# Kernel optimization log

Hardware: AMD Instinct MI355X
Metric: run time of the kernel (lower is better)

Reference implementation:

```python
import jax, jax.numpy as jnp
import numpy as np

B, M, N = 32, 512, 512
XD = YD = 512   # x_size, y_size
S = 512         # shared_size
H = 512         # hidden_size
MAXD = 11       # max relative distance


def _lin(k, i, o):
    lim = float(np.sqrt(6.0 / (i + o)))  # xavier_uniform, gain=1
    return jax.random.uniform(k, (i, o), jnp.float32, -lim, lim)


def setup_inputs() -> dict:
    key = jax.random.key(0)
    ks = jax.random.split(key, 16)
    inp = {
        'prem': jax.random.normal(ks[0], (B, M, YD), jnp.float32),
        'hypo': jax.random.normal(ks[1], (B, N, XD), jnp.float32),
        'prem_mask': jnp.ones((B, M), dtype=bool),
        'hypo_mask': jnp.ones((B, N), dtype=bool),
        # projections
        'Wpx': _lin(ks[2], XD, S), 'bpx': jnp.zeros((S,), jnp.float32),
        'Wpy': _lin(ks[3], YD, S), 'bpy': jnp.zeros((S,), jnp.float32),
        # relative-distance bias embedding (2*max_dist+1, squeezed to scalar)
        'dist_embed': jax.random.normal(ks[4], (2 * MAXD + 1,), jnp.float32),
        # self-attention DeepDot MLP: S -> H -> H
        'Ws1': _lin(ks[5], S, H), 'bs1': jnp.zeros((H,), jnp.float32),
        'Ws2': _lin(ks[6], H, H), 'bs2': jnp.zeros((H,), jnp.float32),
        # cross-attention DeepDot MLP: 2S -> H -> H
        'Wa1': _lin(ks[7], 2 * S, H), 'ba1': jnp.zeros((H,), jnp.float32),
        'Wa2': _lin(ks[8], H, H), 'ba2': jnp.zeros((H,), jnp.float32),
        # compare layer: 4S -> H -> H
        'Wc1': _lin(ks[9], 4 * S, H), 'bc1': jnp.zeros((H,), jnp.float32),
        'Wc2': _lin(ks[10], H, H), 'bc2': jnp.zeros((H,), jnp.float32),
        # aggregate layer: 2H -> H -> H
        'Wg1': _lin(ks[11], 2 * H, H), 'bg1': jnp.zeros((H,), jnp.float32),
        'Wg2': _lin(ks[12], H, H), 'bg2': jnp.zeros((H,), jnp.float32),
    }
    return inp


def _mlp2(x, W1, b1, W2, b2):
    # Linear -> ReLU -> Linear -> ReLU (dropout=0.0)
    h = jax.nn.relu(x @ W1 + b1)
    return jax.nn.relu(h @ W2 + b2)


def _rel_bias(size, dist_embed):
    v = jnp.arange(size)
    d = jnp.clip(v[None, :] - v[:, None], -MAXD, MAXD) + MAXD  # [size,size]
    return dist_embed[d]


def _masked_softmax(t, mask):
    # mask True = valid; broadcast over query dim
    return jax.nn.softmax(jnp.where(mask, t, -jnp.inf), axis=-1)


def reference(prem, hypo, prem_mask, hypo_mask,
              Wpx, bpx, Wpy, bpy, dist_embed,
              Ws1, bs1, Ws2, bs2,
              Wa1, ba1, Wa2, ba2,
              Wc1, bc1, Wc2, bc2,
              Wg1, bg1, Wg2, bg2):
    hypo_p = hypo @ Wpx + bpx   # [B,N,S]
    prem_p = prem @ Wpy + bpy   # [B,M,S]

    # self attention (DeepDot: shared MLP on q and k, then qk^T)
    fp = _mlp2(prem_p, Ws1, bs1, Ws2, bs2)
    fh = _mlp2(hypo_p, Ws1, bs1, Ws2, bs2)
    p_scores = jnp.einsum('bmh,bnh->bmn', fp, fp) + _rel_bias(prem_p.shape[1], dist_embed)[None]
    h_scores = jnp.einsum('bmh,bnh->bmn', fh, fh) + _rel_bias(hypo_p.shape[1], dist_embed)[None]

    p_att = _masked_softmax(p_scores, prem_mask[:, None, :])
    h_att = _masked_softmax(h_scores, hypo_mask[:, None, :])
    prem_ctx = jnp.einsum('bmn,bnd->bmd', p_att, prem_p)
    hypo_ctx = jnp.einsum('bmn,bnd->bmd', h_att, hypo_p)

    prem2 = jnp.concatenate([prem_p, prem_ctx], axis=-1)  # [B,M,2S]
    hypo2 = jnp.concatenate([hypo_p, hypo_ctx], axis=-1)  # [B,N,2S]

    # cross attention
    gp = _mlp2(prem2, Wa1, ba1, Wa2, ba2)
    gh = _mlp2(hypo2, Wa1, ba1, Wa2, ba2)
    sim = jnp.einsum('bmh,bnh->bmn', gp, gh)  # [B,M,N]
    p2h = _masked_softmax(sim, hypo_mask[:, None, :])
    h2p = _masked_softmax(jnp.swapaxes(sim, 1, 2), prem_mask[:, None, :])
    attended_hypo = jnp.einsum('bmn,bnd->bmd', p2h, hypo2)  # [B,M,2S]
    attended_prem = jnp.einsum('bnm,bmd->bnd', h2p, prem2)  # [B,N,2S]

    prem_cmp = _mlp2(jnp.concatenate([prem2, attended_hypo], -1), Wc1, bc1, Wc2, bc2)
    hypo_cmp = _mlp2(jnp.concatenate([hypo2, attended_prem], -1), Wc1, bc1, Wc2, bc2)

    prem_cmp = (prem_cmp * prem_mask[..., None].astype(prem_cmp.dtype)).sum(axis=1)  # [B,H]
    hypo_cmp = (hypo_cmp * hypo_mask[..., None].astype(hypo_cmp.dtype)).sum(axis=1)  # [B,H]

    return _mlp2(jnp.concatenate([prem_cmp, hypo_cmp], -1), Wg1, bg1, Wg2, bg2)
```

## Files before the change

kernel.cpp:

```cpp
#include <hip/hip_runtime.h>
#include <hip/hip_bf16.h>


typedef __bf16 bf16x8 __attribute__((ext_vector_type(8)));
typedef float floatx16 __attribute__((ext_vector_type(16)));
typedef float floatx4 __attribute__((ext_vector_type(4)));

__device__ __forceinline__ unsigned short f32_to_bf16(float f) {
    unsigned int u = __float_as_uint(f);
    unsigned int r = (u + 0x7FFFu + ((u >> 16) & 1u)) >> 16;
    return (unsigned short)r;
}
__device__ __forceinline__ float bf16_to_f32(unsigned short h) {
    return __uint_as_float(((unsigned int)h) << 16);
}

__device__ __forceinline__ void gload16(const void* g, void* l) {
    __builtin_amdgcn_global_load_lds(
        (const __attribute__((address_space(1))) unsigned int*)g,
        (__attribute__((address_space(3))) unsigned int*)l, 16, 0, 0);
}

#define FENCE_BAR() do { asm volatile("" ::: "memory"); \
    __builtin_amdgcn_s_barrier(); \
    asm volatile("" ::: "memory"); } while (0)

struct TW {
    const float* src[8];
    unsigned short* dst[8];
    int K[8];
};
__global__ __launch_bounds__(256) void transpose_all_kernel(TW tw) {
    const int z = blockIdx.z;
    const int K = tw.K[z];
    const int k0 = blockIdx.y * 32;
    if (k0 >= K) return;
    const float* W = tw.src[z];
    unsigned short* Wt = tw.dst[z];
    __shared__ unsigned short tile[32][33];
    int n0 = blockIdx.x * 32;
    int tx = threadIdx.x & 31, ty = threadIdx.x >> 5;
    #pragma unroll
    for (int i = 0; i < 4; ++i) {
        int ky = ty + i * 8;
        tile[ky][tx] = f32_to_bf16(W[(long long)(k0 + ky) * 512 + n0 + tx]);
    }
    __syncthreads();
    #pragma unroll
    for (int i = 0; i < 4; ++i) {
        int ny = ty + i * 8;
        Wt[(long long)(n0 + ny) * K + k0 + tx] = tile[tx][ny];
    }
}

template <bool BT, bool AF32>
__global__ __launch_bounds__(256, 4) void gemm_kernel(
    const void* __restrict__ Av, const void* __restrict__ A2v, int lda, long long strideA,
    const unsigned short* __restrict__ Bw, int ldb, long long strideB, int bxor,
    const unsigned short* __restrict__ B2, const float* __restrict__ bias2, int Msplit,
    float* __restrict__ C32, unsigned short* __restrict__ Cb, int ldc, long long strideC,
    const float* __restrict__ bias, int relu, int M, int N, int K,
    float* __restrict__ csum, int swz) {
    constexpr int BBYTES = BT ? 8192 : (32 * 264);
    constexpr int BUF = 8192 + BBYTES;
    __shared__ alignas(16) char smem[2 * BUF];

    const int t = threadIdx.x;
    const int lane = t & 63;
    const int wave = t >> 6;
    const int wm = (wave >> 1) * 64;
    const int wn = (wave & 1) * 64;
    const int ln = lane & 31;
    const int h = lane >> 5;

    int bx = blockIdx.x, by = blockIdx.y, bz = blockIdx.z;
    if (swz == 1) {
        int Nt = gridDim.x, Mt = gridDim.y;
        int L = by * Nt + bx;
        int x = L & 7, s = L >> 3;
        by = x * (Mt >> 3) + s / Nt;
        bx = s % Nt;
    } else if (swz == 2) {
        int Nt = gridDim.x, Mt = gridDim.y;
        int L = (bz * Mt + by) * Nt + bx;
        int x = L & 7, s = L >> 3;
        int mg = x * ((Mt * (int)gridDim.z) >> 3) + s / Nt;
        bx = s % Nt;
        by = mg % Mt;
        bz = mg / Mt;
    }
    const int m0 = by * 128;
    const int n0 = bx * 128;
    const int bzB = (bz + bxor) & ((int)gridDim.z - 1);

    const unsigned short* B = Bw;
    const float* biasp = bias;
    long long mA = m0;
    if (Msplit && m0 >= Msplit) {
        if (B2) B = B2;
        if (bias2) biasp = bias2;
        if (A2v) { Av = A2v; mA = m0 - Msplit; }
    }

    const float* aptrF = nullptr;
    const unsigned short* aptrH = nullptr;
    if constexpr (AF32)
        aptrF = (const float*)Av + (long long)bz * strideA +
                (mA + (t >> 1)) * (long long)lda + (t & 1) * 16;
    else
        aptrH = (const unsigned short*)Av + (long long)bz * strideA +
                (mA + (t >> 1)) * (long long)lda + (t & 1) * 16;
    const unsigned short* bptr;
    if (BT)
        bptr = B + (long long)bzB * strideB +
               (long long)(n0 + (t >> 1)) * ldb + (t & 1) * 16;
    else
        bptr = B + (long long)bzB * strideB +
               (long long)(t >> 4) * ldb + n0 + (t & 15) * 8;
    const long long bstep = BT ? 8 : 16 * (long long)ldb;

    const int aoff = ((t & 1) * 256 + (t >> 1)) * 16;
    const int boff = BT ? (8192 + ((t & 1) * 256 + (t >> 1)) * 16)
                        : (8192 + (t >> 4) * 264 + (t & 15) * 16);
    const int boff2 = BT ? 2048 : 16 * 264;

    floatx16 acc[2][2];
    #pragma unroll
    for (int im = 0; im < 2; ++im)
        #pragma unroll
        for (int in = 0; in < 2; ++in)
            acc[im][in] = (floatx16)(0.f);

    uint4 va0, va1, vb0, vb1;
    float4 fa0, fa1, fa2, fa3;

    auto loadA = [&]() {
        if constexpr (AF32) {
            fa0 = *(const float4*)(aptrF);
            fa1 = *(const float4*)(aptrF + 4);
            fa2 = *(const float4*)(aptrF + 8);
            fa3 = *(const float4*)(aptrF + 12);
            aptrF += 32;
        } else {
            va0 = *(const uint4*)(aptrH);
            va1 = *(const uint4*)(aptrH + 8);
            aptrH += 32;
        }
    };
    auto loadB = [&]() {
        vb0 = *(const uint4*)(bptr);
        vb1 = *(const uint4*)(bptr + bstep);
        bptr += BT ? 32 : 32 * (long long)ldb;
    };
    auto commit = [&](char* buf) {
        if constexpr (AF32) {
            union { uint4 q; unsigned short u[8]; } c0, c1;
            c0.u[0] = f32_to_bf16(fa0.x); c0.u[1] = f32_to_bf16(fa0.y);
            c0.u[2] = f32_to_bf16(fa0.z); c0.u[3] = f32_to_bf16(fa0.w);
            c0.u[4] = f32_to_bf16(fa1.x); c0.u[5] = f32_to_bf16(fa1.y);
            c0.u[6] = f32_to_bf16(fa1.z); c0.u[7] = f32_to_bf16(fa1.w);
            c1.u[0] = f32_to_bf16(fa2.x); c1.u[1] = f32_to_bf16(fa2.y);
            c1.u[2] = f32_to_bf16(fa2.z); c1.u[3] = f32_to_bf16(fa2.w);
            c1.u[4] = f32_to_bf16(fa3.x); c1.u[5] = f32_to_bf16(fa3.y);
            c1.u[6] = f32_to_bf16(fa3.z); c1.u[7] = f32_to_bf16(fa3.w);
            *(uint4*)(buf + aoff) = c0.q;
            *(uint4*)(buf + aoff + 2048) = c1.q;
        } else {
            *(uint4*)(buf + aoff) = va0;
            *(uint4*)(buf + aoff + 2048) = va1;
        }
        *(uint4*)(buf + boff) = vb0;
        *(uint4*)(buf + boff + boff2) = vb1;
    };

    loadA(); loadB();
    commit(smem);
    loadA(); loadB();
    __syncthreads();

    int p = 0;
    for (int k0 = 0; k0 < K; k0 += 32) {
        const char* base = smem + p * BUF;
        #pragma unroll
        for (int s = 0; s < 2; ++s) {
            bf16x8 a[2], b[2];
            #pragma unroll
            for (int im = 0; im < 2; ++im)
                a[im] = *(const bf16x8*)(base + ((s * 2 + h) * 128 + wm + im * 32 + ln) * 16);
            if (BT) {
                #pragma unroll
                for (int in = 0; in < 2; ++in)
                    b[in] = *(const bf16x8*)(base + 8192 +
                                             ((s * 2 + h) * 128 + wn + in * 32 + ln) * 16);
            } else {
                #pragma unroll
                for (int in = 0; in < 2; ++in) {
                    union { bf16x8 v; unsigned short u[8]; } u;
                    #pragma unroll
                    for (int j = 0; j < 8; ++j)
                        u.u[j] = *(const unsigned short*)(base + 8192 +
                                 (s * 16 + h * 8 + j) * 264 + (wn + in * 32 + ln) * 2);
                    b[in] = u.v;
                }
            }
            #pragma unroll
            for (int im = 0; im < 2; ++im)
                #pragma unroll
                for (int in = 0; in < 2; ++in)
                    acc[im][in] = __builtin_amdgcn_mfma_f32_32x32x16_bf16(
                        a[im], b[in], acc[im][in], 0, 0, 0);
        }

        if (k0 + 32 < K) {
            commit(smem + (p ^ 1) * BUF);
            if (k0 + 64 < K) { loadA(); loadB(); }
            __syncthreads();
            p ^= 1;
        }
    }

    if (csum) {
        const int bidx = m0 >> 9;
        const long long cbase = (long long)(bidx & 31) * 1024 + (bidx >> 5) * 512;
        #pragma unroll
        for (int in = 0; in < 2; ++in) {
            int n = n0 + wn + in * 32 + ln;
            float bn = biasp ? biasp[n] : 0.f;
            float s = 0.f;
            #pragma unroll
            for (int im = 0; im < 2; ++im)
                #pragma unroll
                for (int r = 0; r < 16; ++r) {
                    float v = acc[im][in][r] + bn;
                    if (relu) v = fmaxf(v, 0.f);
                    s += v;
                }
            s += __shfl_xor(s, 32);
            if (lane < 32) atomicAdd(&csum[cbase + n], s);
        }
        return;
    }

    float* C32b = C32 ? C32 + (long long)bz * strideC : nullptr;
    unsigned short* Cbb = Cb ? Cb + (long long)bz * strideC : nullptr;
    #pragma unroll
    for (int im = 0; im < 2; ++im) {
        #pragma unroll
        for (int in = 0; in < 2; ++in) {
            int n = n0 + wn + in * 32 + ln;
            float bn = biasp ? biasp[n] : 0.f;
            #pragma unroll
            for (int r = 0; r < 16; ++r) {
                int m = m0 + wm + im * 32 + (r & 3) + 8 * (r >> 2) + 4 * h;
                float v = acc[im][in][r] + bn;
                if (relu) v = fmaxf(v, 0.f);
                long long off = (long long)m * ldc + n;
                if (C32b) C32b[off] = v;
                if (Cbb) Cbb[off] = f32_to_bf16(v);
            }
        }
    }
}

__global__ __launch_bounds__(512, 2) void gemm256_kernel(
    const unsigned short* __restrict__ Aw, int lda, long long strideA,
    const unsigned short* __restrict__ Bw, int ldb, long long strideB, int bxor,
    float* __restrict__ C32, unsigned short* __restrict__ Cb, int ldc, long long strideC,
    const float* __restrict__ bias, int relu, int K) {
    extern __shared__ __align__(16) char smem[];

    const int tid = threadIdx.x;
    const int lane = tid & 63;
    const int wave = tid >> 6;
    const int wr = wave >> 2;
    const int wc = wave & 3;

    int bx = blockIdx.x, by = blockIdx.y, bz = blockIdx.z;
    {
        const int gx = gridDim.x, gy = gridDim.y;
        const int nwg = gx * gy * (int)gridDim.z;
        if ((nwg & 7) == 0) {
            int L = (bz * gy + by) * gx + bx;
            int flat = (L & 7) * (nwg >> 3) + (L >> 3);
            bx = flat % gx;
            int R = flat / gx;
            by = R % gy;
            bz = R / gy;
        }
    }
    const int m0 = by * 256;
    const int n0 = bx * 256;
    const int bzB = (bz + bxor) & ((int)gridDim.z - 1);

    const int rowT = tid >> 3;
    const int chS = (tid & 7) ^ (rowT & 7);
    const long long ldaB = (long long)lda * 2;
    const long long ldbB = (long long)ldb * 2;
    const char* aG = (const char*)Aw +
        ((long long)bz * strideA + (long long)(m0 + rowT) * lda) * 2 + chS * 16;
    const char* bG = (const char*)Bw +
        ((long long)bzB * strideB + (long long)(n0 + rowT) * ldb) * 2 + chS * 16;
    const int dOff = tid * 16;

    auto stA = [&](int tt, int h) {
        const char* g = aG + (long long)(h * 128) * ldaB + (long long)tt * 128;
        char* l = smem + (tt & 1) * 65536 + h * 16384 + dOff;
        gload16(g, l);
        gload16(g + 64 * ldaB, l + 8192);
    };
    auto stB = [&](int tt, int h) {
        const char* g = bG + (long long)(h * 128) * ldbB + (long long)tt * 128;
        char* l = smem + (tt & 1) * 65536 + 32768 + h * 16384 + dOff;
        gload16(g, l);
        gload16(g + 64 * ldbB, l + 8192);
    };

    const int l15 = lane & 15;
    const int lk = lane >> 4;
    const int swzb = (lane & 7) << 4;
    const int c0 = (lk * 16) ^ swzb;
    const int c1 = (64 + lk * 16) ^ swzb;
    const int arow = (wr * 128 + l15) * 128;
    const int brow = 32768 + (wc * 64 + l15) * 128;

    floatx4 acc[8][4];
    #pragma unroll
    for (int mf = 0; mf < 8; ++mf)
        #pragma unroll
        for (int nf = 0; nf < 4; ++nf)
            acc[mf][nf] = (floatx4)(0.f);

    const int NT = K >> 6;

    stA(0, 0); stA(0, 1); stB(0, 0); stB(0, 1);
    if (NT > 1) {
        stB(1, 0); stB(1, 1);
        asm volatile("s_waitcnt vmcnt(4)" ::: "memory");
    } else {
        asm volatile("s_waitcnt vmcnt(0)" ::: "memory");
    }
    FENCE_BAR();

    bf16x8 a[4][2], b[4][2];
    for (int t = 0; t < NT; ++t) {
        const char* buf = smem + (t & 1) * 65536;
        const char* aB = buf + arow;
        const char* bB = buf + brow;

        #pragma unroll
        for (int mf = 0; mf < 4; ++mf) {
            a[mf][0] = *(const bf16x8*)(aB + mf * 2048 + c0);
            a[mf][1] = *(const bf16x8*)(aB + mf * 2048 + c1);
        }
        #pragma unroll
        for (int nf = 0; nf < 2; ++nf) {
            b[nf][0] = *(const bf16x8*)(bB + nf * 2048 + c0);
            b[nf][1] = *(const bf16x8*)(bB + nf * 2048 + c1);
        }
        if (t + 1 < NT) stA(t + 1, 0);
        FENCE_BAR();
        __builtin_amdgcn_s_setprio(1);
        #pragma unroll
        for (int mf = 0; mf < 4; ++mf)
            #pragma unroll
            for (int nf = 0; nf < 2; ++nf) {
                acc[mf][nf] = __builtin_amdgcn_mfma_f32_16x16x32_bf16(
                    a[mf][0], b[nf][0], acc[mf][nf], 0, 0, 0);
                acc[mf][nf] = __builtin_amdgcn_mfma_f32_16x16x32_bf16(
                    a[mf][1], b[nf][1], acc[mf][nf], 0, 0, 0);
            }
        __builtin_amdgcn_s_setprio(0);
        FENCE_BAR();

        #pragma unroll
        for (int nf = 2; nf < 4; ++nf) {
            b[nf][0] = *(const bf16x8*)(bB + nf * 2048 + c0);
            b[nf][1] = *(const bf16x8*)(bB + nf * 2048 + c1);
        }
        if (t + 1 < NT) stA(t + 1, 1);
        FENCE_BAR();
        __builtin_amdgcn_s_setprio(1);
        #pragma unroll
        for (int mf = 0; mf < 4; ++mf)
            #pragma unroll
            for (int nf = 2; nf < 4; ++nf) {
                acc[mf][nf] = __builtin_amdgcn_mfma_f32_16x16x32_bf16(
                    a[mf][0], b[nf][0], acc[mf][nf], 0, 0, 0);
                acc[mf][nf] = __builtin_amdgcn_mfma_f32_16x16x32_bf16(
                    a[mf][1], b[nf][1], acc[mf][nf], 0, 0, 0);
            }
        __builtin_amdgcn_s_setprio(0);
        FENCE_BAR();

        #pragma unroll
        for (int mf = 0; mf < 4; ++mf) {
            a[mf][0] = *(const bf16x8*)(aB + (4 + mf) * 2048 + c0);
            a[mf][1] = *(const bf16x8*)(aB + (4 + mf) * 2048 + c1);
        }
        if (t + 2 < NT) stB(t + 2, 0);
        FENCE_BAR();
        __builtin_amdgcn_s_setprio(1);
        #pragma unroll
        for (int mf = 0; mf < 4; ++mf)
            #pragma unroll
            for (int nf = 2; nf < 4; ++nf) {
                acc[4 + mf][nf] = __builtin_amdgcn_mfma_f32_16x16x32_bf16(
                    a[mf][0], b[nf][0], acc[4 + mf][nf], 0, 0, 0);
                acc[4 + mf][nf] = __builtin_amdgcn_mfma_f32_16x16x32_bf16(
                    a[mf][1], b[nf][1], acc[4 + mf][nf], 0, 0, 0);
            }
        __builtin_amdgcn_s_setprio(0);
        FENCE_BAR();

        if (t + 2 < NT) {
            stB(t + 2, 1);
            asm volatile("s_waitcnt vmcnt(4)" ::: "memory");
        } else {
            asm volatile("s_waitcnt vmcnt(0)" ::: "memory");
        }
        FENCE_BAR();
        __builtin_amdgcn_s_setprio(1);
        #pragma unroll
        for (int mf = 0; mf < 4; ++mf)
            #pragma unroll
            for (int nf = 0; nf < 2; ++nf) {
                acc[4 + mf][nf] = __builtin_amdgcn_mfma_f32_16x16x32_bf16(
                    a[mf][0], b[nf][0], acc[4 + mf][nf], 0, 0, 0);
                acc[4 + mf][nf] = __builtin_amdgcn_mfma_f32_16x16x32_bf16(
                    a[mf][1], b[nf][1], acc[4 + mf][nf], 0, 0, 0);
            }
        __builtin_amdgcn_s_setprio(0);
        FENCE_BAR();
    }

    const int rg = (lane >> 4) * 4;
    float* C32b = C32 ? C32 + (long long)bz * strideC : nullptr;
    unsigned short* Cbb = Cb ? Cb + (long long)bz * strideC : nullptr;
    #pragma unroll
    for (int nf = 0; nf < 4; ++nf) {
        const int n = n0 + wc * 64 + nf * 16 + l15;
        const float bn = bias ? bias[n] : 0.f;
        #pragma unroll
        for (int mf = 0; mf < 8; ++mf) {
            #pragma unroll
            for (int r = 0; r < 4; ++r) {
                int m = m0 + wr * 128 + mf * 16 + rg + r;
                float v = acc[mf][nf][r] + bn;
                if (relu) v = fmaxf(v, 0.f);
                long long off = (long long)m * ldc + n;
                if (C32b) C32b[off] = v;
                if (Cbb) Cbb[off] = f32_to_bf16(v);
            }
        }
    }
}

__global__ __launch_bounds__(256) void softmax_kernel(const float* S,
                                                      unsigned short* P,
                                                      const float* de, int rel) {
    const int row = blockIdx.x;
    const int b = blockIdx.y;
    const long long baseS = ((long long)b * 512 + row) * 512;
    const long long baseP = ((long long)b * 512 + row) * 1024;
    const int t = threadIdx.x;
    const int lane = t & 63, wv = t >> 6;
    __shared__ float redmax[4], redsum[4];

    float v[2];
    float mx = -1e30f;
    #pragma unroll
    for (int i = 0; i < 2; ++i) {
        int c = t + i * 256;
        float x = S[baseS + c];
        if (rel) {
            int d = c - row;
            d = min(11, max(-11, d));
            x += de[d + 11];
        }
        v[i] = x;
        mx = fmaxf(mx, x);
    }
    #pragma unroll
    for (int o = 32; o > 0; o >>= 1) mx = fmaxf(mx, __shfl_down(mx, o));
    if (lane == 0) redmax[wv] = mx;
    __syncthreads();
    mx = fmaxf(fmaxf(redmax[0], redmax[1]), fmaxf(redmax[2], redmax[3]));

    float s = 0.f;
    #pragma unroll
    for (int i = 0; i < 2; ++i) { v[i] = __expf(v[i] - mx); s += v[i]; }
    #pragma unroll
    for (int o = 32; o > 0; o >>= 1) s += __shfl_down(s, o);
    if (lane == 0) redsum[wv] = s;
    __syncthreads();
    s = redsum[0] + redsum[1] + redsum[2] + redsum[3];
    float inv = 1.f / s;
    #pragma unroll
    for (int i = 0; i < 2; ++i) P[baseP + t + i * 256] = f32_to_bf16(v[i] * inv);
}

__global__ __launch_bounds__(512) void mlp_agg_kernel(const float* __restrict__ X,
                                                      const float* __restrict__ W,
                                                      const float* __restrict__ bias,
                                                      float* __restrict__ out,
                                                      int K, int N, int relu) {
    const int b = blockIdx.y;
    const int nl = threadIdx.x & 63;
    const int n = blockIdx.x * 64 + nl;
    const int ks = threadIdx.x >> 6;
    const int kchunk = K >> 3;
    const float* Xb = X + (long long)b * K;
    const int k0 = ks * kchunk;
    float s = 0.f;
    #pragma unroll 8
    for (int k = k0; k < k0 + kchunk; ++k)
        s += Xb[k] * W[(long long)k * N + n];
    __shared__ float red[8][64];
    red[ks][nl] = s;
    __syncthreads();
    if (threadIdx.x < 64) {
        float t = 0.f;
        #pragma unroll
        for (int i = 0; i < 8; ++i) t += red[i][threadIdx.x];
        t += bias[n];
        if (relu) t = fmaxf(t, 0.f);
        out[(long long)b * N + n] = t;
    }
}

static void gemm(hipStream_t st, bool bt, bool af32,
                 const void* A, const void* A2, int lda, long long sA,
                 const void* B, int ldb, long long sB, int bxor,
                 const void* B2, const float* bias2, int Msplit,
                 float* C32, void* Cb, int ldc, long long sC,
                 const float* bias, int relu, int M, int N, int K, int batch,
                 float* csum = nullptr) {
    dim3 g(N / 128, M / 128, batch), blk(256);
    int swz = 0;
    if (batch == 1 && (M / 128) % 8 == 0) swz = 1;
    else if (batch > 1 && ((M / 128) * batch) % 8 == 0) swz = 2;
    if (bt) {
        if (af32)
            gemm_kernel<true, true><<<g, blk, 0, st>>>(
                A, A2, lda, sA, (const unsigned short*)B, ldb, sB, bxor,
                (const unsigned short*)B2, bias2, Msplit,
                C32, (unsigned short*)Cb, ldc, sC, bias, relu, M, N, K, csum, swz);
        else
            gemm_kernel<true, false><<<g, blk, 0, st>>>(
                A, A2, lda, sA, (const unsigned short*)B, ldb, sB, bxor,
                (const unsigned short*)B2, bias2, Msplit,
                C32, (unsigned short*)Cb, ldc, sC, bias, relu, M, N, K, csum, swz);
    } else {
        gemm_kernel<false, false><<<g, blk, 0, st>>>(
            A, A2, lda, sA, (const unsigned short*)B, ldb, sB, bxor,
            (const unsigned short*)B2, bias2, Msplit,
            C32, (unsigned short*)Cb, ldc, sC, bias, relu, M, N, K, csum, swz);
    }
}

static void gemm256(hipStream_t st,
                    const void* A, int lda, long long sA,
                    const void* B, int ldb, long long sB, int bxor,
                    float* C32, void* Cb, int ldc, long long sC,
                    const float* bias, int relu, int M, int N, int K, int batch) {
    static bool inited = false;
    if (!inited) {
        hipFuncSetAttribute(reinterpret_cast<const void*>(gemm256_kernel),
                            hipFuncAttributeMaxDynamicSharedMemorySize, 131072);
        inited = true;
    }
    dim3 g(N / 256, M / 256, batch);
    gemm256_kernel<<<g, 512, 131072, st>>>(
        (const unsigned short*)A, lda, sA,
        (const unsigned short*)B, ldb, sB, bxor,
        C32, (unsigned short*)Cb, ldc, sC, bias, relu, K);
}

extern "C" void kernel_launch(void* const* d_in, const int* in_sizes, int n_in,
                              void* d_out, int out_size, void* d_ws, size_t ws_size,
                              hipStream_t stream) {
    const int B = 32, SEQ = 512;
    const int MT = B * SEQ;
    const int M2 = 2 * MT;

    const float* prem = (const float*)d_in[0];
    const float* hypo = (const float*)d_in[1];
    const float* Wpx = (const float*)d_in[4];  const float* bpx = (const float*)d_in[5];
    const float* Wpy = (const float*)d_in[6];  const float* bpy = (const float*)d_in[7];
    const float* de  = (const float*)d_in[8];
    const float* Ws1 = (const float*)d_in[9];  const float* bs1 = (const float*)d_in[10];
    const float* Ws2 = (const float*)d_in[11]; const float* bs2 = (const float*)d_in[12];
    const float* Wa1 = (const float*)d_in[13]; const float* ba1 = (const float*)d_in[14];
    const float* Wa2 = (const float*)d_in[15]; const float* ba2 = (const float*)d_in[16];
    const float* Wc1 = (const float*)d_in[17]; const float* bc1 = (const float*)d_in[18];
    const float* Wc2 = (const float*)d_in[19]; const float* bc2 = (const float*)d_in[20];
    const float* Wg1 = (const float*)d_in[21]; const float* bg1 = (const float*)d_in[22];
    const float* Wg2 = (const float*)d_in[23]; const float* bg2 = (const float*)d_in[24];

    char* p = (char*)d_ws;
    auto alloc = [&](size_t bytes) { char* r = p; p += (bytes + 255) & ~(size_t)255; return r; };
    unsigned short* prem_bf = (unsigned short*)alloc((size_t)MT * 512 * 2);
    unsigned short* hypo_bf = (unsigned short*)alloc((size_t)MT * 512 * 2);
    unsigned short* premcat = (unsigned short*)alloc((size_t)MT * 2048 * 2);
    unsigned short* hypocat = (unsigned short*)alloc((size_t)MT * 2048 * 2);
    float* scores = (float*)alloc((size_t)64 * SEQ * SEQ * 4);
    unsigned short* h1 = (unsigned short*)scores;
    unsigned short* att = (unsigned short*)scores;
    unsigned short* Wpx_t = (unsigned short*)alloc(512 * 512 * 2);
    unsigned short* Wpy_t = (unsigned short*)alloc(512 * 512 * 2);
    unsigned short* Ws1_t = (unsigned short*)alloc(512 * 512 * 2);
    unsigned short* Ws2_t = (unsigned short*)alloc(512 * 512 * 2);
    unsigned short* Wa1_t = (unsigned short*)alloc(512 * 1024 * 2);
    unsigned short* Wa2_t = (unsigned short*)alloc(512 * 512 * 2);
    unsigned short* Wc1_t = (unsigned short*)alloc(512 * 2048 * 2);
    unsigned short* Wc2_t = (unsigned short*)alloc(512 * 512 * 2);
    float* agg  = (float*)alloc(32 * 1024 * 4);
    float* aggh = (float*)alloc(32 * 512 * 4);
    (void)hypo_bf; (void)hypocat;

    const long long sBM = (long long)SEQ * SEQ;
    const long long sAtt = (long long)SEQ * 1024;
    const long long sCat = (long long)SEQ * 2048;

    {
        TW tw;
        tw.src[0] = Wpy; tw.dst[0] = Wpy_t; tw.K[0] = 512;
        tw.src[1] = Wpx; tw.dst[1] = Wpx_t; tw.K[1] = 512;
        tw.src[2] = Ws1; tw.dst[2] = Ws1_t; tw.K[2] = 512;
        tw.src[3] = Ws2; tw.dst[3] = Ws2_t; tw.K[3] = 512;
        tw.src[4] = Wa1; tw.dst[4] = Wa1_t; tw.K[4] = 1024;
        tw.src[5] = Wa2; tw.dst[5] = Wa2_t; tw.K[5] = 512;
        tw.src[6] = Wc1; tw.dst[6] = Wc1_t; tw.K[6] = 2048;
        tw.src[7] = Wc2; tw.dst[7] = Wc2_t; tw.K[7] = 512;
        transpose_all_kernel<<<dim3(16, 64, 8), 256, 0, stream>>>(tw);
        hipMemsetAsync(agg, 0, 32 * 1024 * sizeof(float), stream);
    }

    gemm(stream, true, true, prem, hypo, 512, 0, Wpy_t, 512, 0, 0,
         Wpx_t, bpx, MT, nullptr, premcat, 2048, 0, bpy, 0, M2, 512, 512, 1);

    gemm256(stream, premcat, 2048, 0, Ws1_t, 512, 0, 0,
            nullptr, h1, 512, 0, bs1, 1, M2, 512, 512, 1);
    gemm256(stream, h1, 512, 0, Ws2_t, 512, 0, 0,
            nullptr, prem_bf, 512, 0, bs2, 1, M2, 512, 512, 1);

    gemm(stream, true, false, prem_bf, nullptr, 512, sBM, prem_bf, 512, sBM, 0,
         nullptr, nullptr, 0, scores, nullptr, 512, sBM, nullptr, 0, 512, 512, 512, 64);
    softmax_kernel<<<dim3(512, 64), 256, 0, stream>>>(scores, att, de, 1);
    gemm(stream, false, false, att, nullptr, 1024, sAtt, premcat, 2048, sCat, 0,
         nullptr, nullptr, 0, nullptr, premcat + 512, 2048, sCat, nullptr, 0, 512, 512, 512, 64);

    gemm256(stream, premcat, 2048, 0, Wa1_t, 1024, 0, 0,
            nullptr, h1, 512, 0, ba1, 1, M2, 512, 1024, 1);
    gemm256(stream, h1, 512, 0, Wa2_t, 512, 0, 0,
            nullptr, prem_bf, 512, 0, ba2, 1, M2, 512, 512, 1);

    gemm(stream, true, false, prem_bf, nullptr, 512, sBM, prem_bf, 512, sBM, 32,
         nullptr, nullptr, 0, scores, nullptr, 512, sBM, nullptr, 0, 512, 512, 512, 64);
    softmax_kernel<<<dim3(512, 64), 256, 0, stream>>>(scores, att, de, 0);
    gemm(stream, false, false, att, nullptr, 1024, sAtt, premcat, 2048, sCat, 32,
         nullptr, nullptr, 0, nullptr, premcat + 1024, 2048, sCat, nullptr, 0, 512, 1024, 512, 64);

    gemm256(stream, premcat, 2048, 0, Wc1_t, 2048, 0, 0,
            nullptr, h1, 512, 0, bc1, 1, M2, 512, 2048, 1);
    gemm(stream, true, false, h1, nullptr, 512, 0, Wc2_t, 512, 0, 0,
         nullptr, nullptr, 0, nullptr, nullptr, 512, 0, bc2, 1, M2, 512, 512, 1, agg);

    mlp_agg_kernel<<<dim3(8, 32), 512, 0, stream>>>(agg, Wg1, bg1, aggh, 1024, 512, 1);
    mlp_agg_kernel<<<dim3(8, 32), 512, 0, stream>>>(aggh, Wg2, bg2, (float*)d_out, 512, 512, 1);
}
```

Before: 645.4 us.

## Fuse score GEMM with relative bias and softmax into one attention kernel

```diff
diff --git a/kernel.cpp b/kernel.cpp
--- a/kernel.cpp
+++ b/kernel.cpp
@@ -453,6 +453,163 @@
             }
         }
     }
+}
+
+__global__ __launch_bounds__(256, 2) void attn_kernel(
+    const unsigned short* __restrict__ F,
+    int bxor,
+    unsigned short* __restrict__ att,
+    const float* __restrict__ de, int rel) {
+    constexpr int BUF = 36864;
+    __shared__ alignas(16) char smem[2 * BUF];
+    __shared__ alignas(16) float red[2][64][4];
+    __shared__ float deL[23];
+
+    const int t = threadIdx.x;
+    const int lane = t & 63;
+    const int wave = t >> 6;
+    const int ln = lane & 31;
+    const int h = lane >> 5;
+
+    const int by = blockIdx.x;
+    const int bz = blockIdx.y;
+    const int m0 = by * 64;
+    const int bzB = (bz + bxor) & 63;
+
+    if (t < 23) deL[t] = de[t];
+
+    const unsigned short* aptr = F + (long long)bz * (512 * 512) +
+                                 (m0 + (t >> 2)) * 512 + (t & 3) * 8;
+    const unsigned short* bptr = F + (long long)bzB * (512 * 512) +
+                                 (t >> 1) * 512 + (t & 1) * 16;
+    const int aoff = ((t & 3) * 64 + (t >> 2)) * 16;
+    const int c2 = (t & 1) * 2;
+    const int brow = (t >> 1) * 16;
+
+    floatx16 acc[2][4];
+    #pragma unroll
+    for (int mf = 0; mf < 2; ++mf)
+        #pragma unroll
+        for (int nf = 0; nf < 4; ++nf)
+            acc[mf][nf] = (floatx16)(0.f);
+
+    uint4 qa, q0a, q0b, q1a, q1b, q2a, q2b, q3a, q3b;
+    auto load = [&]() {
+        qa  = *(const uint4*)(aptr);
+        q0a = *(const uint4*)(bptr);
+        q0b = *(const uint4*)(bptr + 8);
+        q1a = *(const uint4*)(bptr + 65536);
+        q1b = *(const uint4*)(bptr + 65536 + 8);
+        q2a = *(const uint4*)(bptr + 131072);
+        q2b = *(const uint4*)(bptr + 131072 + 8);
+        q3a = *(const uint4*)(bptr + 196608);
+        q3b = *(const uint4*)(bptr + 196608 + 8);
+        aptr += 32; bptr += 32;
+    };
+    auto commit = [&](char* buf) {
+        *(uint4*)(buf + aoff) = qa;
+        char* bb = buf + 4096;
+        *(uint4*)(bb + (c2 + 0) * 8192 + brow) = q0a;
+        *(uint4*)(bb + (c2 + 1) * 8192 + brow) = q0b;
+        *(uint4*)(bb + (c2 + 0) * 8192 + brow + 128 * 16) = q1a;
+        *(uint4*)(bb + (c2 + 1) * 8192 + brow + 128 * 16) = q1b;
+        *(uint4*)(bb + (c2 + 0) * 8192 + brow + 256 * 16) = q2a;
+        *(uint4*)(bb + (c2 + 1) * 8192 + brow + 256 * 16) = q2b;
+        *(uint4*)(bb + (c2 + 0) * 8192 + brow + 384 * 16) = q3a;
+        *(uint4*)(bb + (c2 + 1) * 8192 + brow + 384 * 16) = q3b;
+    };
+
+    load(); commit(smem); load();
+    __syncthreads();
+
+    int p = 0;
+    for (int k0 = 0; k0 < 512; k0 += 32) {
+        const char* buf = smem + p * BUF;
+        #pragma unroll
+        for (int s = 0; s < 2; ++s) {
+            bf16x8 a[2], b[4];
+            #pragma unroll
+            for (int mf = 0; mf < 2; ++mf)
+                a[mf] = *(const bf16x8*)(buf + ((s * 2 + h) * 64 + mf * 32 + ln) * 16);
+            #pragma unroll
+            for (int nf = 0; nf < 4; ++nf)
+                b[nf] = *(const bf16x8*)(buf + 4096 + (s * 2 + h) * 8192 +
+                                         (wave * 128 + nf * 32 + ln) * 16);
+            #pragma unroll
+            for (int mf = 0; mf < 2; ++mf)
+                #pragma unroll
+                for (int nf = 0; nf < 4; ++nf)
+                    acc[mf][nf] = __builtin_amdgcn_mfma_f32_32x32x16_bf16(
+                        a[mf], b[nf], acc[mf][nf], 0, 0, 0);
+        }
+        if (k0 + 32 < 512) {
+            commit(smem + (p ^ 1) * BUF);
+            if (k0 + 64 < 512) load();
+            __syncthreads();
+            p ^= 1;
+        }
+    }
+
+    if (rel) {
+        #pragma unroll
+        for (int mf = 0; mf < 2; ++mf)
+            #pragma unroll
+            for (int nf = 0; nf < 4; ++nf)
+                #pragma unroll
+                for (int r = 0; r < 16; ++r) {
+                    int row = m0 + mf * 32 + (r & 3) + 8 * (r >> 2) + 4 * h;
+                    int col = wave * 128 + nf * 32 + ln;
+                    int d = min(11, max(-11, col - row));
+                    acc[mf][nf][r] += deL[d + 11];
+                }
+    }
+
+    #pragma unroll
+    for (int mf = 0; mf < 2; ++mf)
+        #pragma unroll
+        for (int r = 0; r < 16; ++r) {
+            float mx = fmaxf(fmaxf(acc[mf][0][r], acc[mf][1][r]),
+                             fmaxf(acc[mf][2][r], acc[mf][3][r]));
+            #pragma unroll
+            for (int o = 16; o > 0; o >>= 1) mx = fmaxf(mx, __shfl_xor(mx, o));
+            if (ln == 0)
+                red[0][mf * 32 + (r & 3) + 8 * (r >> 2) + 4 * h][wave] = mx;
+        }
+    __syncthreads();
+
+    #pragma unroll
+    for (int mf = 0; mf < 2; ++mf)
+        #pragma unroll
+        for (int r = 0; r < 16; ++r) {
+            const int rl = mf * 32 + (r & 3) + 8 * (r >> 2) + 4 * h;
+            float4 q = *(const float4*)red[0][rl];
+            float mx = fmaxf(fmaxf(q.x, q.y), fmaxf(q.z, q.w));
+            float s = 0.f;
+            #pragma unroll
+            for (int nf = 0; nf < 4; ++nf) {
+                acc[mf][nf][r] = __expf(acc[mf][nf][r] - mx);
+                s += acc[mf][nf][r];
+            }
+            #pragma unroll
+            for (int o = 16; o > 0; o >>= 1) s += __shfl_xor(s, o);
+            if (ln == 0) red[1][rl][wave] = s;
+        }
+    __syncthreads();
+
+    unsigned short* ab = att + ((long long)bz * 512 + m0) * 1024;
+    #pragma unroll
+    for (int mf = 0; mf < 2; ++mf)
+        #pragma unroll
+        for (int r = 0; r < 16; ++r) {
+            const int rl = mf * 32 + (r & 3) + 8 * (r >> 2) + 4 * h;
+            float4 q = *(const float4*)red[1][rl];
+            float inv = 1.f / (q.x + q.y + q.z + q.w);
+            #pragma unroll
+            for (int nf = 0; nf < 4; ++nf) {
+                int col = wave * 128 + nf * 32 + ln;
+                ab[(long long)rl * 1024 + col] = f32_to_bf16(acc[mf][nf][r] * inv);
+            }
+        }
 }
 
 __global__ __launch_bounds__(256) void softmax_kernel(const float* S,
@@ -616,7 +773,7 @@
     unsigned short* Wc2_t = (unsigned short*)alloc(512 * 512 * 2);
     float* agg  = (float*)alloc(32 * 1024 * 4);
     float* aggh = (float*)alloc(32 * 512 * 4);
-    (void)hypo_bf; (void)hypocat;
+    (void)hypo_bf; (void)hypocat; (void)scores;
 
     const long long sBM = (long long)SEQ * SEQ;
     const long long sAtt = (long long)SEQ * 1024;
@@ -644,9 +801,7 @@
     gemm256(stream, h1, 512, 0, Ws2_t, 512, 0, 0,
             nullptr, prem_bf, 512, 0, bs2, 1, M2, 512, 512, 1);
 
-    gemm(stream, true, false, prem_bf, nullptr, 512, sBM, prem_bf, 512, sBM, 0,
-         nullptr, nullptr, 0, scores, nullptr, 512, sBM, nullptr, 0, 512, 512, 512, 64);
-    softmax_kernel<<<dim3(512, 64), 256, 0, stream>>>(scores, att, de, 1);
+    attn_kernel<<<dim3(8, 64), 256, 0, stream>>>(prem_bf, 0, att, de, 1);
     gemm(stream, false, false, att, nullptr, 1024, sAtt, premcat, 2048, sCat, 0,
          nullptr, nullptr, 0, nullptr, premcat + 512, 2048, sCat, nullptr, 0, 512, 512, 512, 64);
 
@@ -655,9 +810,7 @@
     gemm256(stream, h1, 512, 0, Wa2_t, 512, 0, 0,
             nullptr, prem_bf, 512, 0, ba2, 1, M2, 512, 512, 1);
 
-    gemm(stream, true, false, prem_bf, nullptr, 512, sBM, prem_bf, 512, sBM, 32,
-         nullptr, nullptr, 0, scores, nullptr, 512, sBM, nullptr, 0, 512, 512, 512, 64);
-    softmax_kernel<<<dim3(512, 64), 256, 0, stream>>>(scores, att, de, 0);
+    attn_kernel<<<dim3(8, 64), 256, 0, stream>>>(prem_bf, 32, att, de, 0);
     gemm(stream, false, false, att, nullptr, 1024, sAtt, premcat, 2048, sCat, 32,
          nullptr, nullptr, 0, nullptr, premcat + 1024, 2048, sCat, nullptr, 0, 512, 1024, 512, 64);
 
```

Measured after the change: 681.9 us. +5.7%, slower.
